# Kernel tuning notes

Measured on AMD Instinct MI355X. Metric: run time of the kernel, lower is better.

Reference implementation:

```python
import jax, jax.numpy as jnp
import numpy as np
from itertools import combinations

B, M = 128, 24
EMB = 16
NEG_SLOPE = 0.01  # torch F.leaky_relu default


def _combo_index():
    # 60 combinations: choose 2 of 4 hole cards x choose 3 of 5 board cards.
    hero = list(combinations(range(4), 2))      # 6
    board = list(combinations(range(5), 3))     # 10
    combos = []
    for h in hero:
        for b in board:
            combos.append([h[0], h[1], 4 + b[0], 4 + b[1], 4 + b[2]])
    return np.asarray(combos, dtype=np.int32)   # (60, 5)

_COMBOS = jnp.asarray(_combo_index())


def setup_inputs() -> dict:
    key = jax.random.key(0)
    ks = jax.random.split(key, 12)
    ranks = jax.random.randint(ks[0], (B, M, 9), 1, 14)   # 1..13
    suits = jax.random.randint(ks[1], (B, M, 9), 1, 5)    # 1..4
    x = jnp.stack([ranks, suits], axis=-1).reshape(B, M, 18).astype(jnp.int64)

    def lin(k, fan_in, fan_out):
        bound = 1.0 / np.sqrt(fan_in)
        kw, kb = jax.random.split(k)
        W = jax.random.uniform(kw, (fan_in, fan_out), minval=-bound, maxval=bound, dtype=jnp.float32)
        b = jax.random.uniform(kb, (fan_out,), minval=-bound, maxval=bound, dtype=jnp.float32)
        return W, b

    card_emb = jax.random.normal(ks[2], (53, EMB), dtype=jnp.float32)
    card_emb = card_emb.at[0].set(0.0)  # padding_idx=0
    hand_W, hand_b = lin(ks[3], 32, 128)
    board_W, board_b = lin(ks[4], 48, 128)
    hidden_W, hidden_b = lin(ks[5], 256, 256)
    out_W, out_b = lin(ks[6], 60 * 256, 256)
    return {"x": x, "card_emb": card_emb,
            "hand_W": hand_W, "hand_b": hand_b,
            "board_W": board_W, "board_b": board_b,
            "hidden_W": hidden_W, "hidden_b": hidden_b,
            "out_W": out_W, "out_b": out_b}


def reference(x, card_emb, hand_W, hand_b, board_W, board_b,
              hidden_W, hidden_b, out_W, out_b):
    act = lambda v: jax.nn.leaky_relu(v, NEG_SLOPE)
    Bx, Mx = x.shape[0], x.shape[1]
    ranks = x[..., 0::2]                       # (B,M,9)
    suits = x[..., 1::2]
    rc = jnp.take(ranks, _COMBOS, axis=-1)     # (B,M,60,5)
    sc = jnp.take(suits, _COMBOS, axis=-1)
    rc = jnp.where(rc > 0, rc - 1, 0)          # ranks -> 0..12
    sc = jnp.where(sc > 0, (sc - 1) * 13, 0)   # suit offset 0/13/26/39
    cards = rc + sc                            # (B,M,60,5) in [0,52)
    emb = card_emb[cards]                      # (B,M,60,5,16)
    hero = emb[..., :2, :].reshape(Bx, Mx, 60, 32)
    board = emb[..., 2:, :].reshape(Bx, Mx, 60, 48)
    hero = act(hero @ hand_W + hand_b)         # (B,M,60,128)
    board = act(board @ board_W + board_b)     # (B,M,60,128)
    h = act(jnp.concatenate([hero, board], axis=-1) @ hidden_W + hidden_b)  # (B,M,60,256)
    flat = h.reshape(Bx, Mx, 60 * 256)         # (B,M,15360)
    return act(flat @ out_W + out_b)           # (B,M,256)
```

## Files before the change

### kernel.cpp

```cpp
#include <hip/hip_runtime.h>
#include <hip/hip_bf16.h>
#include <cstdint>
#include <cstddef>

typedef __hip_bfloat16 bf16;
typedef __attribute__((ext_vector_type(8))) short short8;
typedef __attribute__((ext_vector_type(4))) float floatx4;

#define KO 15360
#define KS 12
#define KSLICE 1280

__device__ __forceinline__ float lrelu(float v) { return v > 0.f ? v : 0.01f * v; }

__device__ __forceinline__ float bflo(unsigned int u) {
  unsigned int x = u << 16; float f; __builtin_memcpy(&f, &x, 4); return f;
}
__device__ __forceinline__ float bfhi(unsigned int u) {
  unsigned int x = u & 0xffff0000u; float f; __builtin_memcpy(&f, &x, 4); return f;
}
__device__ __forceinline__ unsigned int pk2(float lo, float hi) {
  bf16 a = __float2bfloat16(lo), b = __float2bfloat16(hi);
  unsigned short ua, ub;
  __builtin_memcpy(&ua, &a, 2); __builtin_memcpy(&ub, &b, 2);
  return (unsigned int)ua | ((unsigned int)ub << 16);
}
__device__ __forceinline__ unsigned int hpair(unsigned int u, unsigned int v) {
  return pk2(lrelu(bflo(u) + bflo(v)), lrelu(bfhi(u) + bfhi(v)));
}

__device__ __forceinline__ void async_lds16(const bf16* g, bf16* l) {
  __builtin_amdgcn_global_load_lds((__attribute__((address_space(1))) void*)(g),
                                   (__attribute__((address_space(3))) void*)(l),
                                   16, 0, 0);
}

__global__ __launch_bounds__(256) void transpose_k(const float* __restrict__ W,
                                                   bf16* __restrict__ Wt, int K)
{
  __shared__ float tile[64][65];
  const int kb = blockIdx.x * 64;
  const int nb = blockIdx.y * 64;
  const int t = threadIdx.x;
  #pragma unroll
  for (int i = 0; i < 16; ++i) {
    int idx = t + 256 * i;
    int r = idx >> 6, c = idx & 63;
    tile[r][c] = W[(size_t)(kb + r) * 256 + nb + c];
  }
  __syncthreads();
  #pragma unroll
  for (int i = 0; i < 16; ++i) {
    int idx = t + 256 * i;
    int r = idx >> 6, c = idx & 63;
    Wt[(size_t)(nb + r) * K + kb + c] = __float2bfloat16(tile[c][r]);
  }
}

__global__ __launch_bounds__(256) void hb_pack(
    const int* __restrict__ x, const float* __restrict__ card_emb,
    const float* __restrict__ hand_W, const float* __restrict__ hand_b,
    const float* __restrict__ board_W, const float* __restrict__ board_b,
    bf16* __restrict__ Abuf)
{
  static constexpr int H0[6] = {0,0,0,1,1,2};
  static constexpr int H1[6] = {1,2,3,2,3,3};
  static constexpr int B0[10] = {0,0,0,0,0,0,1,1,1,2};
  static constexpr int B1[10] = {1,1,1,2,2,3,2,2,3,3};
  static constexpr int B2[10] = {2,3,4,3,4,4,3,4,4,4};

  __shared__ float wH[32 * 128];
  __shared__ float wB[48 * 128];
  __shared__ float bH[128], bB[128];
  __shared__ float emb[4][9][16];
  __shared__ bf16 At[2][16][264];

  const int t = threadIdx.x;
  const int item0 = blockIdx.x * 4;

  for (int i = t; i < 32 * 128; i += 256) wH[i] = hand_W[i];
  for (int i = t; i < 48 * 128; i += 256) wB[i] = board_W[i];
  if (t < 128) { bH[t] = hand_b[t]; bB[t] = board_b[t]; }
  for (int ii = t; ii < 576; ii += 256) {
    int li = ii / 144, idx = ii - li * 144;
    int ci = idx >> 4, e = idx & 15;
    int rk = x[(item0 + li) * 18 + 2 * ci], st = x[(item0 + li) * 18 + 2 * ci + 1];
    int card = (rk > 0 ? rk - 1 : 0) + (st > 0 ? (st - 1) * 13 : 0);
    emb[li][ci][e] = card_emb[card * 16 + e];
  }
  __syncthreads();

  const int half = t >> 7, j = t & 127;

  for (int pass = 0; pass < 2; ++pass) {
    const int embi = 2 * pass + half;
    {
      bf16 z = __float2bfloat16(0.f);
      #pragma unroll
      for (int p = 0; p < 6; ++p) At[half][p][128 + j] = z;
      #pragma unroll
      for (int b = 0; b < 10; ++b) At[half][6 + b][j] = z;
    }
    float aH[6], aB[10];
    {
      float hb = bH[j], bb = bB[j];
      #pragma unroll
      for (int p = 0; p < 6; ++p) aH[p] = hb;
      #pragma unroll
      for (int b = 0; b < 10; ++b) aB[b] = bb;
    }
    #pragma unroll
    for (int k = 0; k < 16; ++k) {
      float e[9];
      #pragma unroll
      for (int c = 0; c < 9; ++c) e[c] = emb[embi][c][k];
      float w0 = wH[k * 128 + j], w1 = wH[(16 + k) * 128 + j];
      float v0 = wB[k * 128 + j], v1 = wB[(16 + k) * 128 + j], v2 = wB[(32 + k) * 128 + j];
      #pragma unroll
      for (int p = 0; p < 6; ++p)
        aH[p] += e[H0[p]] * w0 + e[H1[p]] * w1;
      #pragma unroll
      for (int b = 0; b < 10; ++b)
        aB[b] += e[4 + B0[b]] * v0 + e[4 + B1[b]] * v1 + e[4 + B2[b]] * v2;
    }
    #pragma unroll
    for (int p = 0; p < 6; ++p) At[half][p][j] = __float2bfloat16(lrelu(aH[p]));
    #pragma unroll
    for (int b = 0; b < 10; ++b) At[half][6 + b][128 + j] = __float2bfloat16(lrelu(aB[b]));
    __syncthreads();

    #pragma unroll
    for (int li2 = 0; li2 < 2; ++li2) {
      #pragma unroll
      for (int cc = 0; cc < 2; ++cc) {
        int c = t + 256 * cc;
        int m = c & 15, kq = (c >> 4) & 3, ks = c >> 6;
        short8 v = *(const short8*)&At[li2][m][ks * 32 + kq * 8];
        *(short8*)(Abuf + (size_t)(item0 + 2 * pass + li2) * 4096 + (size_t)c * 8) = v;
      }
    }
    __syncthreads();
  }
}

__global__ __launch_bounds__(256, 2) void uv_gemm(
    const bf16* __restrict__ Abuf, const bf16* __restrict__ hWt,
    const float* __restrict__ hidden_b, bf16* __restrict__ UV)
{
  const int t = threadIdx.x, w = t >> 6, l = t & 63;
  const int lr = l & 15, quad = l >> 4;

  short8 bfrag[4][8];
  float bias[4];
  #pragma unroll
  for (int tl = 0; tl < 4; ++tl) {
    int n = w * 64 + tl * 16 + lr;
    bias[tl] = hidden_b[n];
    #pragma unroll
    for (int ks = 0; ks < 8; ++ks)
      bfrag[tl][ks] = *(const short8*)(hWt + (size_t)n * 256 + ks * 32 + quad * 8);
  }

  const int i0 = blockIdx.x * 6;
  for (int ii = 0; ii < 6; ++ii) {
    const bf16* ab = Abuf + (size_t)(i0 + ii) * 4096;
    short8 a[8];
    #pragma unroll
    for (int ks = 0; ks < 8; ++ks)
      a[ks] = *(const short8*)(ab + (size_t)(ks * 64 + l) * 8);

    floatx4 acc[4];
    floatx4 zero = {0.f, 0.f, 0.f, 0.f};
    #pragma unroll
    for (int i = 0; i < 4; ++i) acc[i] = zero;
    #pragma unroll
    for (int ks = 0; ks < 8; ++ks)
      #pragma unroll
      for (int tl = 0; tl < 4; ++tl)
        acc[tl] = __builtin_amdgcn_mfma_f32_16x16x32_bf16(a[ks], bfrag[tl][ks], acc[tl], 0, 0, 0);

    bf16* dst = UV + (size_t)(i0 + ii) * 4096;
    #pragma unroll
    for (int tl = 0; tl < 4; ++tl) {
      int n = w * 64 + tl * 16 + lr;
      #pragma unroll
      for (int r = 0; r < 4; ++r) {
        int m = quad * 4 + r;
        float v = acc[tl][r] + (m >= 6 ? bias[tl] : 0.f);
        dst[m * 256 + n] = __float2bfloat16(v);
      }
    }
  }
}

__global__ __launch_bounds__(256, 2) void out_gemm(
    const bf16* __restrict__ UV, const bf16* __restrict__ Wt,
    float* __restrict__ pbuf)
{
  __shared__ bf16 As[64 * 64];
  __shared__ bf16 Bs[256 * 64];

  const int t = threadIdx.x;
  const int w = t >> 6, l = t & 63, lr = l & 15, quad = l >> 4;
  const int m0 = blockIdx.x * 64;
  const int ks0 = blockIdx.y * KSLICE;
  const int ar = t >> 2, ac = t & 3;

  const bf16* rowp[8];
  {
    int rl = l >> 3, j = (l & 7) ^ rl;
    #pragma unroll
    for (int q = 0; q < 8; ++q)
      rowp[q] = Wt + (size_t)(w * 64 + 8 * q + rl) * KO + ks0 + j * 8;
  }
  bf16* BsW = &Bs[w * 4096];

  floatx4 acc[16];
  floatx4 zero = {0.f, 0.f, 0.f, 0.f};
  #pragma unroll
  for (int i = 0; i < 16; ++i) acc[i] = zero;

  uint4 cu0, cu1, cv0, cv1;
  {
    const int combo = ks0 >> 8;
    const int urow = combo / 10, vrow = 6 + (combo - urow * 10);
    const int c0 = ks0 & 255;
    const bf16* ub = UV + ((size_t)(m0 + ar) * 16 + urow) * 256 + c0 + ac * 16;
    const bf16* vb = UV + ((size_t)(m0 + ar) * 16 + vrow) * 256 + c0 + ac * 16;
    cu0 = *(const uint4*)ub;  cu1 = *(const uint4*)(ub + 8);
    cv0 = *(const uint4*)vb;  cv1 = *(const uint4*)(vb + 8);
  }

  for (int it = 0; it < KSLICE / 64; ++it) {
    __syncthreads();

    #pragma unroll
    for (int q = 0; q < 8; ++q)
      async_lds16(rowp[q] + it * 64, BsW + q * 512);

    {
      uint4 h0, h1;
      h0.x = hpair(cu0.x, cv0.x); h0.y = hpair(cu0.y, cv0.y);
      h0.z = hpair(cu0.z, cv0.z); h0.w = hpair(cu0.w, cv0.w);
      h1.x = hpair(cu1.x, cv1.x); h1.y = hpair(cu1.y, cv1.y);
      h1.z = hpair(cu1.z, cv1.z); h1.w = hpair(cu1.w, cv1.w);
      int jA0 = (2 * ac) ^ (ar & 7);
      int jA1 = (2 * ac + 1) ^ (ar & 7);
      *(uint4*)&As[ar * 64 + jA0 * 8] = h0;
      *(uint4*)&As[ar * 64 + jA1 * 8] = h1;
    }

    __syncthreads();

    if (it + 1 < KSLICE / 64) {
      const int gk2 = ks0 + (it + 1) * 64;
      const int combo = gk2 >> 8;
      const int urow = combo / 10, vrow = 6 + (combo - urow * 10);
      const int c0 = gk2 & 255;
      const bf16* ub = UV + ((size_t)(m0 + ar) * 16 + urow) * 256 + c0 + ac * 16;
      const bf16* vb = UV + ((size_t)(m0 + ar) * 16 + vrow) * 256 + c0 + ac * 16;
      cu0 = *(const uint4*)ub;  cu1 = *(const uint4*)(ub + 8);
      cv0 = *(const uint4*)vb;  cv1 = *(const uint4*)(vb + 8);
    }

    #pragma unroll
    for (int ks = 0; ks < 2; ++ks) {
      short8 af[4], bfr[4];
      #pragma unroll
      for (int i = 0; i < 4; ++i) {
        int row = i * 16 + lr;
        int jp = (4 * ks + quad) ^ (row & 7);
        af[i] = *(const short8*)&As[row * 64 + jp * 8];
      }
      #pragma unroll
      for (int j = 0; j < 4; ++j) {
        int row = w * 64 + j * 16 + lr;
        int jp = (4 * ks + quad) ^ (row & 7);
        bfr[j] = *(const short8*)&Bs[row * 64 + jp * 8];
      }
      #pragma unroll
      for (int i = 0; i < 4; ++i)
        #pragma unroll
        for (int j = 0; j < 4; ++j)
          acc[i * 4 + j] = __builtin_amdgcn_mfma_f32_16x16x32_bf16(af[i], bfr[j], acc[i * 4 + j], 0, 0, 0);
    }
  }

  float* dst = pbuf + (((size_t)blockIdx.y * 48 + blockIdx.x) * 4 + w) * 4096 + l;
  #pragma unroll
  for (int a = 0; a < 16; ++a)
    #pragma unroll
    for (int r = 0; r < 4; ++r)
      dst[(a * 4 + r) * 64] = acc[a][r];
}

__global__ __launch_bounds__(256) void reduce_bias(
    const float* __restrict__ pbuf, const float* __restrict__ outb,
    float* __restrict__ out, int slice_stride)
{
  int idx = blockIdx.x * 256 + threadIdx.x;
  float s = 0.f;
  #pragma unroll
  for (int k = 0; k < KS; ++k) s += pbuf[idx + (size_t)k * slice_stride];
  int l = idx & 63, q = (idx >> 6) & 63, w = (idx >> 12) & 3, bx = idx >> 14;
  int a = q >> 2, r = q & 3, i = a >> 2, tl = a & 3;
  int lr = l & 15, quad = l >> 4;
  int m = bx * 64 + i * 16 + quad * 4 + r;
  int n = w * 64 + tl * 16 + lr;
  out[(size_t)m * 256 + n] = lrelu(s + outb[n]);
}

extern "C" void kernel_launch(void* const* d_in, const int* in_sizes, int n_in,
                              void* d_out, int out_size, void* d_ws, size_t ws_size,
                              hipStream_t stream)
{
  const int*   x        = (const int*)  d_in[0];
  const float* card_emb = (const float*)d_in[1];
  const float* hand_W   = (const float*)d_in[2];
  const float* hand_b   = (const float*)d_in[3];
  const float* board_W  = (const float*)d_in[4];
  const float* board_b  = (const float*)d_in[5];
  const float* hidden_W = (const float*)d_in[6];
  const float* hidden_b = (const float*)d_in[7];
  const float* out_W    = (const float*)d_in[8];
  const float* out_b    = (const float*)d_in[9];
  float* out = (float*)d_out;

  const int NI = in_sizes[0] / 18;

  char* ws = (char*)d_ws;
  bf16* hWt  = (bf16*)ws;
  bf16* oWt  = (bf16*)(ws + 131072);
  bf16* UV   = (bf16*)(ws + 131072 + 7864320);
  bf16* Abuf = (bf16*)(ws + 131072 + 7864320 + (size_t)NI * 8192);
  float* pbuf = (float*)Abuf;

  transpose_k<<<dim3(4, 4),   256, 0, stream>>>(hidden_W, hWt, 256);
  transpose_k<<<dim3(240, 4), 256, 0, stream>>>(out_W,    oWt, KO);
  hb_pack<<<NI / 4, 256, 0, stream>>>(x, card_emb, hand_W, hand_b,
                                      board_W, board_b, Abuf);
  uv_gemm<<<NI / 6, 256, 0, stream>>>(Abuf, hWt, hidden_b, UV);
  out_gemm<<<dim3(NI / 64, KS), 256, 0, stream>>>(UV, oWt, pbuf);
  reduce_bias<<<NI, 256, 0, stream>>>(pbuf, out_b, out, NI * 256);
}
```

Measured before the change: 180.7 us.

## Fuse hand/board pack with UV GEMM, double-buffer out GEMM, vectorise reduce

Merges the hand/board embedding kernel with the hidden-layer UV GEMM so the packed activations feed MFMAs directly from LDS and skip a global round trip. The output GEMM gets double-buffered LDS tiles, so the next B tile and A build overlap the current MFMAs, and the split-K count goes from 12 to 16 slices. The reduction kernel now handles four elements per thread with float4 loads and stores. Costs are more LDS in out_gemm, since the doubled buffers cut occupancy, and more partial sums to reduce.

```diff
diff --git a/kernel.cpp b/kernel.cpp
--- a/kernel.cpp
+++ b/kernel.cpp
@@ -8,8 +8,9 @@
 typedef __attribute__((ext_vector_type(4))) float floatx4;
 
 #define KO 15360
-#define KS 12
-#define KSLICE 1280
+#define KS 16
+#define KSLICE 960
+#define NIT (KSLICE / 64)
 
 __device__ __forceinline__ float lrelu(float v) { return v > 0.f ? v : 0.01f * v; }
 
@@ -57,11 +58,12 @@
   }
 }
 
-__global__ __launch_bounds__(256) void hb_pack(
+__global__ __launch_bounds__(256, 2) void hb_uv(
     const int* __restrict__ x, const float* __restrict__ card_emb,
     const float* __restrict__ hand_W, const float* __restrict__ hand_b,
     const float* __restrict__ board_W, const float* __restrict__ board_b,
-    bf16* __restrict__ Abuf)
+    const bf16* __restrict__ hWt, const float* __restrict__ hidden_b,
+    bf16* __restrict__ UV)
 {
   static constexpr int H0[6] = {0,0,0,1,1,2};
   static constexpr int H1[6] = {1,2,3,2,3,3};
@@ -76,10 +78,22 @@
   __shared__ bf16 At[2][16][264];
 
   const int t = threadIdx.x;
+  const int w = t >> 6, l = t & 63, lr = l & 15, quad = l >> 4;
   const int item0 = blockIdx.x * 4;
 
-  for (int i = t; i < 32 * 128; i += 256) wH[i] = hand_W[i];
-  for (int i = t; i < 48 * 128; i += 256) wB[i] = board_W[i];
+  short8 bfrag[4][8];
+  float bias[4];
+  #pragma unroll
+  for (int tl = 0; tl < 4; ++tl) {
+    int n = w * 64 + tl * 16 + lr;
+    bias[tl] = hidden_b[n];
+    #pragma unroll
+    for (int ks = 0; ks < 8; ++ks)
+      bfrag[tl][ks] = *(const short8*)(hWt + (size_t)n * 256 + ks * 32 + quad * 8);
+  }
+
+  for (int i = t * 4; i < 4096; i += 1024) *(float4*)&wH[i] = *(const float4*)&hand_W[i];
+  for (int i = t * 4; i < 6144; i += 1024) *(float4*)&wB[i] = *(const float4*)&board_W[i];
   if (t < 128) { bH[t] = hand_b[t]; bB[t] = board_b[t]; }
   for (int ii = t; ii < 576; ii += 256) {
     int li = ii / 144, idx = ii - li * 144;
@@ -93,6 +107,7 @@
   const int half = t >> 7, j = t & 127;
 
   for (int pass = 0; pass < 2; ++pass) {
+    if (pass) __syncthreads();
     const int embi = 2 * pass + half;
     {
       bf16 z = __float2bfloat16(0.f);
@@ -130,75 +145,71 @@
     __syncthreads();
 
     #pragma unroll
-    for (int li2 = 0; li2 < 2; ++li2) {
-      #pragma unroll
-      for (int cc = 0; cc < 2; ++cc) {
-        int c = t + 256 * cc;
-        int m = c & 15, kq = (c >> 4) & 3, ks = c >> 6;
-        short8 v = *(const short8*)&At[li2][m][ks * 32 + kq * 8];
-        *(short8*)(Abuf + (size_t)(item0 + 2 * pass + li2) * 4096 + (size_t)c * 8) = v;
+    for (int li = 0; li < 2; ++li) {
+      short8 a[8];
+      #pragma unroll
+      for (int ks = 0; ks < 8; ++ks)
+        a[ks] = *(const short8*)&At[li][lr][ks * 32 + quad * 8];
+
+      floatx4 acc[4];
+      floatx4 zero = {0.f, 0.f, 0.f, 0.f};
+      #pragma unroll
+      for (int i = 0; i < 4; ++i) acc[i] = zero;
+      #pragma unroll
+      for (int ks = 0; ks < 8; ++ks)
+        #pragma unroll
+        for (int tl = 0; tl < 4; ++tl)
+          acc[tl] = __builtin_amdgcn_mfma_f32_16x16x32_bf16(a[ks], bfrag[tl][ks], acc[tl], 0, 0, 0);
+
+      bf16* dst = UV + (size_t)(item0 + 2 * pass + li) * 4096;
+      #pragma unroll
+      for (int tl = 0; tl < 4; ++tl) {
+        int n = w * 64 + tl * 16 + lr;
+        #pragma unroll
+        for (int r = 0; r < 4; ++r) {
+          int m = quad * 4 + r;
+          float v = acc[tl][r] + (m >= 6 ? bias[tl] : 0.f);
+          dst[m * 256 + n] = __float2bfloat16(v);
+        }
       }
     }
-    __syncthreads();
-  }
-}
-
-__global__ __launch_bounds__(256, 2) void uv_gemm(
-    const bf16* __restrict__ Abuf, const bf16* __restrict__ hWt,
-    const float* __restrict__ hidden_b, bf16* __restrict__ UV)
-{
-  const int t = threadIdx.x, w = t >> 6, l = t & 63;
-  const int lr = l & 15, quad = l >> 4;
-
-  short8 bfrag[4][8];
-  float bias[4];
-  #pragma unroll
-  for (int tl = 0; tl < 4; ++tl) {
-    int n = w * 64 + tl * 16 + lr;
-    bias[tl] = hidden_b[n];
-    #pragma unroll
-    for (int ks = 0; ks < 8; ++ks)
-      bfrag[tl][ks] = *(const short8*)(hWt + (size_t)n * 256 + ks * 32 + quad * 8);
-  }
-
-  const int i0 = blockIdx.x * 6;
-  for (int ii = 0; ii < 6; ++ii) {
-    const bf16* ab = Abuf + (size_t)(i0 + ii) * 4096;
-    short8 a[8];
-    #pragma unroll
-    for (int ks = 0; ks < 8; ++ks)
-      a[ks] = *(const short8*)(ab + (size_t)(ks * 64 + l) * 8);
-
-    floatx4 acc[4];
-    floatx4 zero = {0.f, 0.f, 0.f, 0.f};
-    #pragma unroll
-    for (int i = 0; i < 4; ++i) acc[i] = zero;
-    #pragma unroll
-    for (int ks = 0; ks < 8; ++ks)
-      #pragma unroll
-      for (int tl = 0; tl < 4; ++tl)
-        acc[tl] = __builtin_amdgcn_mfma_f32_16x16x32_bf16(a[ks], bfrag[tl][ks], acc[tl], 0, 0, 0);
-
-    bf16* dst = UV + (size_t)(i0 + ii) * 4096;
-    #pragma unroll
-    for (int tl = 0; tl < 4; ++tl) {
-      int n = w * 64 + tl * 16 + lr;
-      #pragma unroll
-      for (int r = 0; r < 4; ++r) {
-        int m = quad * 4 + r;
-        float v = acc[tl][r] + (m >= 6 ? bias[tl] : 0.f);
-        dst[m * 256 + n] = __float2bfloat16(v);
-      }
-    }
-  }
+  }
+}
+
+__device__ __forceinline__ void uv_fetch(const bf16* __restrict__ UV, int m0, int ar,
+                                         int ac, int ks0, int it,
+                                         uint4& u0, uint4& u1, uint4& v0, uint4& v1)
+{
+  const int gk = ks0 + it * 64;
+  const int combo = gk >> 8;
+  const int urow = combo / 10, vrow = 6 + (combo - urow * 10);
+  const int c0 = gk & 255;
+  const bf16* ub = UV + ((size_t)(m0 + ar) * 16 + urow) * 256 + c0 + ac * 16;
+  const bf16* vb = UV + ((size_t)(m0 + ar) * 16 + vrow) * 256 + c0 + ac * 16;
+  u0 = *(const uint4*)ub;  u1 = *(const uint4*)(ub + 8);
+  v0 = *(const uint4*)vb;  v1 = *(const uint4*)(vb + 8);
+}
+
+__device__ __forceinline__ void build_As(bf16* __restrict__ AsBuf, int ar, int ac,
+                                         uint4 u0, uint4 u1, uint4 v0, uint4 v1)
+{
+  uint4 h0, h1;
+  h0.x = hpair(u0.x, v0.x); h0.y = hpair(u0.y, v0.y);
+  h0.z = hpair(u0.z, v0.z); h0.w = hpair(u0.w, v0.w);
+  h1.x = hpair(u1.x, v1.x); h1.y = hpair(u1.y, v1.y);
+  h1.z = hpair(u1.z, v1.z); h1.w = hpair(u1.w, v1.w);
+  int jA0 = (2 * ac) ^ (ar & 7);
+  int jA1 = (2 * ac + 1) ^ (ar & 7);
+  *(uint4*)&AsBuf[ar * 64 + jA0 * 8] = h0;
+  *(uint4*)&AsBuf[ar * 64 + jA1 * 8] = h1;
 }
 
 __global__ __launch_bounds__(256, 2) void out_gemm(
     const bf16* __restrict__ UV, const bf16* __restrict__ Wt,
     float* __restrict__ pbuf)
 {
-  __shared__ bf16 As[64 * 64];
-  __shared__ bf16 Bs[256 * 64];
+  __shared__ bf16 As[2][64 * 64];
+  __shared__ bf16 Bs[2][256 * 64];
 
   const int t = threadIdx.x;
   const int w = t >> 6, l = t & 63, lr = l & 15, quad = l >> 4;
@@ -213,54 +224,34 @@
     for (int q = 0; q < 8; ++q)
       rowp[q] = Wt + (size_t)(w * 64 + 8 * q + rl) * KO + ks0 + j * 8;
   }
-  bf16* BsW = &Bs[w * 4096];
 
   floatx4 acc[16];
   floatx4 zero = {0.f, 0.f, 0.f, 0.f};
   #pragma unroll
   for (int i = 0; i < 16; ++i) acc[i] = zero;
 
-  uint4 cu0, cu1, cv0, cv1;
+  #pragma unroll
+  for (int q = 0; q < 8; ++q)
+    async_lds16(rowp[q], &Bs[0][w * 4096 + q * 512]);
   {
-    const int combo = ks0 >> 8;
-    const int urow = combo / 10, vrow = 6 + (combo - urow * 10);
-    const int c0 = ks0 & 255;
-    const bf16* ub = UV + ((size_t)(m0 + ar) * 16 + urow) * 256 + c0 + ac * 16;
-    const bf16* vb = UV + ((size_t)(m0 + ar) * 16 + vrow) * 256 + c0 + ac * 16;
-    cu0 = *(const uint4*)ub;  cu1 = *(const uint4*)(ub + 8);
-    cv0 = *(const uint4*)vb;  cv1 = *(const uint4*)(vb + 8);
-  }
-
-  for (int it = 0; it < KSLICE / 64; ++it) {
+    uint4 u0, u1, v0, v1;
+    uv_fetch(UV, m0, ar, ac, ks0, 0, u0, u1, v0, v1);
+    build_As(As[0], ar, ac, u0, u1, v0, v1);
+  }
+  uint4 nu0, nu1, nv0, nv1;
+  uv_fetch(UV, m0, ar, ac, ks0, 1, nu0, nu1, nv0, nv1);
+
+  for (int it = 0; it < NIT; ++it) {
+    const int cur = it & 1, nxt = cur ^ 1;
     __syncthreads();
 
-    #pragma unroll
-    for (int q = 0; q < 8; ++q)
-      async_lds16(rowp[q] + it * 64, BsW + q * 512);
-
-    {
-      uint4 h0, h1;
-      h0.x = hpair(cu0.x, cv0.x); h0.y = hpair(cu0.y, cv0.y);
-      h0.z = hpair(cu0.z, cv0.z); h0.w = hpair(cu0.w, cv0.w);
-      h1.x = hpair(cu1.x, cv1.x); h1.y = hpair(cu1.y, cv1.y);
-      h1.z = hpair(cu1.z, cv1.z); h1.w = hpair(cu1.w, cv1.w);
-      int jA0 = (2 * ac) ^ (ar & 7);
-      int jA1 = (2 * ac + 1) ^ (ar & 7);
-      *(uint4*)&As[ar * 64 + jA0 * 8] = h0;
-      *(uint4*)&As[ar * 64 + jA1 * 8] = h1;
-    }
-
-    __syncthreads();
-
-    if (it + 1 < KSLICE / 64) {
-      const int gk2 = ks0 + (it + 1) * 64;
-      const int combo = gk2 >> 8;
-      const int urow = combo / 10, vrow = 6 + (combo - urow * 10);
-      const int c0 = gk2 & 255;
-      const bf16* ub = UV + ((size_t)(m0 + ar) * 16 + urow) * 256 + c0 + ac * 16;
-      const bf16* vb = UV + ((size_t)(m0 + ar) * 16 + vrow) * 256 + c0 + ac * 16;
-      cu0 = *(const uint4*)ub;  cu1 = *(const uint4*)(ub + 8);
-      cv0 = *(const uint4*)vb;  cv1 = *(const uint4*)(vb + 8);
+    if (it + 1 < NIT) {
+      #pragma unroll
+      for (int q = 0; q < 8; ++q)
+        async_lds16(rowp[q] + (it + 1) * 64, &Bs[nxt][w * 4096 + q * 512]);
+      build_As(As[nxt], ar, ac, nu0, nu1, nv0, nv1);
+      if (it + 2 < NIT)
+        uv_fetch(UV, m0, ar, ac, ks0, it + 2, nu0, nu1, nv0, nv1);
     }
 
     #pragma unroll
@@ -270,13 +261,13 @@
       for (int i = 0; i < 4; ++i) {
         int row = i * 16 + lr;
         int jp = (4 * ks + quad) ^ (row & 7);
-        af[i] = *(const short8*)&As[row * 64 + jp * 8];
+        af[i] = *(const short8*)&As[cur][row * 64 + jp * 8];
       }
       #pragma unroll
       for (int j = 0; j < 4; ++j) {
         int row = w * 64 + j * 16 + lr;
         int jp = (4 * ks + quad) ^ (row & 7);
-        bfr[j] = *(const short8*)&Bs[row * 64 + jp * 8];
+        bfr[j] = *(const short8*)&Bs[cur][row * 64 + jp * 8];
       }
       #pragma unroll
       for (int i = 0; i < 4; ++i)
@@ -298,16 +289,24 @@
     const float* __restrict__ pbuf, const float* __restrict__ outb,
     float* __restrict__ out, int slice_stride)
 {
-  int idx = blockIdx.x * 256 + threadIdx.x;
-  float s = 0.f;
-  #pragma unroll
-  for (int k = 0; k < KS; ++k) s += pbuf[idx + (size_t)k * slice_stride];
-  int l = idx & 63, q = (idx >> 6) & 63, w = (idx >> 12) & 3, bx = idx >> 14;
+  int i4 = blockIdx.x * 256 + threadIdx.x;
+  int idx = i4 * 4;
+  float4 s = *(const float4*)&pbuf[idx];
+  #pragma unroll
+  for (int k = 1; k < KS; ++k) {
+    float4 v = *(const float4*)&pbuf[idx + (size_t)k * slice_stride];
+    s.x += v.x; s.y += v.y; s.z += v.z; s.w += v.w;
+  }
+  int l = idx & 63, q = (idx >> 6) & 63, w2 = (idx >> 12) & 3, bx = idx >> 14;
   int a = q >> 2, r = q & 3, i = a >> 2, tl = a & 3;
   int lr = l & 15, quad = l >> 4;
   int m = bx * 64 + i * 16 + quad * 4 + r;
-  int n = w * 64 + tl * 16 + lr;
-  out[(size_t)m * 256 + n] = lrelu(s + outb[n]);
+  int n = w2 * 64 + tl * 16 + lr;
+  float4 b = *(const float4*)&outb[n];
+  float4 rr;
+  rr.x = lrelu(s.x + b.x); rr.y = lrelu(s.y + b.y);
+  rr.z = lrelu(s.z + b.z); rr.w = lrelu(s.w + b.w);
+  *(float4*)&out[(size_t)m * 256 + n] = rr;
 }
 
 extern "C" void kernel_launch(void* const* d_in, const int* in_sizes, int n_in,
@@ -332,14 +331,12 @@
   bf16* hWt  = (bf16*)ws;
   bf16* oWt  = (bf16*)(ws + 131072);
   bf16* UV   = (bf16*)(ws + 131072 + 7864320);
-  bf16* Abuf = (bf16*)(ws + 131072 + 7864320 + (size_t)NI * 8192);
-  float* pbuf = (float*)Abuf;
+  float* pbuf = (float*)(ws + 131072 + 7864320 + (size_t)NI * 8192);
 
   transpose_k<<<dim3(4, 4),   256, 0, stream>>>(hidden_W, hWt, 256);
   transpose_k<<<dim3(240, 4), 256, 0, stream>>>(out_W,    oWt, KO);
-  hb_pack<<<NI / 4, 256, 0, stream>>>(x, card_emb, hand_W, hand_b,
-                                      board_W, board_b, Abuf);
-  uv_gemm<<<NI / 6, 256, 0, stream>>>(Abuf, hWt, hidden_b, UV);
+  hb_uv<<<NI / 4, 256, 0, stream>>>(x, card_emb, hand_W, hand_b,
+                                    board_W, board_b, hWt, hidden_b, UV);
   out_gemm<<<dim3(NI / 64, KS), 256, 0, stream>>>(UV, oWt, pbuf);
-  reduce_bias<<<NI, 256, 0, stream>>>(pbuf, out_b, out, NI * 256);
-}
+  reduce_bias<<<NI / 4, 256, 0, stream>>>(pbuf, out_b, out, NI * 256);
+}
```

After: 218.3 us. 20.8% more time.

## Retune split-K, swizzle out_gemm blocks, prepack hidden weights, vectorize loads and reduce

Applied to the files above, without the earlier changes.

The output GEMM now uses 16 K-slices of 960 instead of 12 of 1280, on a flattened 1D grid. Block indices are remapped so neighbouring blocks share M tiles across K-slices, which should improve L2 reuse of UV and the weights. The hidden weights are prepacked straight into the MFMA fragment layout, so uv_gemm gets contiguous per-lane loads. hb_pack weight staging uses float4 loads, and the split-K reduction reads, biases and writes four floats per thread. In exchange, the partial-sum buffer grows and there is more reduction traffic, and the new block count may give a worse wave tail on the CUs.

```diff
diff --git a/kernel.cpp b/kernel.cpp
--- a/kernel.cpp
+++ b/kernel.cpp
@@ -8,8 +8,9 @@
 typedef __attribute__((ext_vector_type(4))) float floatx4;
 
 #define KO 15360
-#define KS 12
-#define KSLICE 1280
+#define KS 16
+#define KSLICE 960
+#define NIT (KSLICE / 64)
 
 __device__ __forceinline__ float lrelu(float v) { return v > 0.f ? v : 0.01f * v; }
 
@@ -57,6 +58,29 @@
   }
 }
 
+__global__ __launch_bounds__(256) void pack_hidden(const float* __restrict__ W,
+                                                   bf16* __restrict__ P)
+{
+  __shared__ float Lt[4096];
+  const int g = blockIdx.x, t = threadIdx.x;
+  for (int i = t; i < 4096; i += 256)
+    Lt[i] = W[(size_t)(i >> 4) * 256 + g * 16 + (i & 15)];
+  __syncthreads();
+  #pragma unroll
+  for (int cc = 0; cc < 2; ++cc) {
+    int c = t + 256 * cc;
+    int ks = c >> 6, l = c & 63, lr = l & 15, quad = l >> 4;
+    short8 v;
+    #pragma unroll
+    for (int j = 0; j < 8; ++j) {
+      bf16 b = __float2bfloat16(Lt[(ks * 32 + quad * 8 + j) * 16 + lr]);
+      short s; __builtin_memcpy(&s, &b, 2);
+      v[j] = s;
+    }
+    *(short8*)(P + ((size_t)(g * 8 + ks) * 64 + l) * 8) = v;
+  }
+}
+
 __global__ __launch_bounds__(256) void hb_pack(
     const int* __restrict__ x, const float* __restrict__ card_emb,
     const float* __restrict__ hand_W, const float* __restrict__ hand_b,
@@ -78,8 +102,8 @@
   const int t = threadIdx.x;
   const int item0 = blockIdx.x * 4;
 
-  for (int i = t; i < 32 * 128; i += 256) wH[i] = hand_W[i];
-  for (int i = t; i < 48 * 128; i += 256) wB[i] = board_W[i];
+  for (int i = t * 4; i < 4096; i += 1024) *(float4*)&wH[i] = *(const float4*)&hand_W[i];
+  for (int i = t * 4; i < 6144; i += 1024) *(float4*)&wB[i] = *(const float4*)&board_W[i];
   if (t < 128) { bH[t] = hand_b[t]; bB[t] = board_b[t]; }
   for (int ii = t; ii < 576; ii += 256) {
     int li = ii / 144, idx = ii - li * 144;
@@ -93,6 +117,7 @@
   const int half = t >> 7, j = t & 127;
 
   for (int pass = 0; pass < 2; ++pass) {
+    if (pass) __syncthreads();
     const int embi = 2 * pass + half;
     {
       bf16 z = __float2bfloat16(0.f);
@@ -144,7 +169,7 @@
 }
 
 __global__ __launch_bounds__(256, 2) void uv_gemm(
-    const bf16* __restrict__ Abuf, const bf16* __restrict__ hWt,
+    const bf16* __restrict__ Abuf, const bf16* __restrict__ hWtp,
     const float* __restrict__ hidden_b, bf16* __restrict__ UV)
 {
   const int t = threadIdx.x, w = t >> 6, l = t & 63;
@@ -154,11 +179,10 @@
   float bias[4];
   #pragma unroll
   for (int tl = 0; tl < 4; ++tl) {
-    int n = w * 64 + tl * 16 + lr;
-    bias[tl] = hidden_b[n];
+    bias[tl] = hidden_b[w * 64 + tl * 16 + lr];
     #pragma unroll
     for (int ks = 0; ks < 8; ++ks)
-      bfrag[tl][ks] = *(const short8*)(hWt + (size_t)n * 256 + ks * 32 + quad * 8);
+      bfrag[tl][ks] = *(const short8*)(hWtp + ((size_t)((w * 4 + tl) * 8 + ks) * 64 + l) * 8);
   }
 
   const int i0 = blockIdx.x * 6;
@@ -193,6 +217,20 @@
   }
 }
 
+__device__ __forceinline__ void uv_fetch(const bf16* __restrict__ UV, int m0, int ar,
+                                         int ac, int ks0, int it,
+                                         uint4& u0, uint4& u1, uint4& v0, uint4& v1)
+{
+  const int gk = ks0 + it * 64;
+  const int combo = gk >> 8;
+  const int urow = combo / 10, vrow = 6 + (combo - urow * 10);
+  const int c0 = gk & 255;
+  const bf16* ub = UV + ((size_t)(m0 + ar) * 16 + urow) * 256 + c0 + ac * 16;
+  const bf16* vb = UV + ((size_t)(m0 + ar) * 16 + vrow) * 256 + c0 + ac * 16;
+  u0 = *(const uint4*)ub;  u1 = *(const uint4*)(ub + 8);
+  v0 = *(const uint4*)vb;  v1 = *(const uint4*)(vb + 8);
+}
+
 __global__ __launch_bounds__(256, 2) void out_gemm(
     const bf16* __restrict__ UV, const bf16* __restrict__ Wt,
     float* __restrict__ pbuf)
@@ -201,9 +239,12 @@
   __shared__ bf16 Bs[256 * 64];
 
   const int t = threadIdx.x;
+  const int id = blockIdx.x;
+  const int by = ((id & 7) << 1) | ((id >> 3) & 1);
+  const int bx = id >> 4;
   const int w = t >> 6, l = t & 63, lr = l & 15, quad = l >> 4;
-  const int m0 = blockIdx.x * 64;
-  const int ks0 = blockIdx.y * KSLICE;
+  const int m0 = bx * 64;
+  const int ks0 = by * KSLICE;
   const int ar = t >> 2, ac = t & 3;
 
   const bf16* rowp[8];
@@ -221,17 +262,9 @@
   for (int i = 0; i < 16; ++i) acc[i] = zero;
 
   uint4 cu0, cu1, cv0, cv1;
-  {
-    const int combo = ks0 >> 8;
-    const int urow = combo / 10, vrow = 6 + (combo - urow * 10);
-    const int c0 = ks0 & 255;
-    const bf16* ub = UV + ((size_t)(m0 + ar) * 16 + urow) * 256 + c0 + ac * 16;
-    const bf16* vb = UV + ((size_t)(m0 + ar) * 16 + vrow) * 256 + c0 + ac * 16;
-    cu0 = *(const uint4*)ub;  cu1 = *(const uint4*)(ub + 8);
-    cv0 = *(const uint4*)vb;  cv1 = *(const uint4*)(vb + 8);
-  }
-
-  for (int it = 0; it < KSLICE / 64; ++it) {
+  uv_fetch(UV, m0, ar, ac, ks0, 0, cu0, cu1, cv0, cv1);
+
+  for (int it = 0; it < NIT; ++it) {
     __syncthreads();
 
     #pragma unroll
@@ -252,16 +285,8 @@
 
     __syncthreads();
 
-    if (it + 1 < KSLICE / 64) {
-      const int gk2 = ks0 + (it + 1) * 64;
-      const int combo = gk2 >> 8;
-      const int urow = combo / 10, vrow = 6 + (combo - urow * 10);
-      const int c0 = gk2 & 255;
-      const bf16* ub = UV + ((size_t)(m0 + ar) * 16 + urow) * 256 + c0 + ac * 16;
-      const bf16* vb = UV + ((size_t)(m0 + ar) * 16 + vrow) * 256 + c0 + ac * 16;
-      cu0 = *(const uint4*)ub;  cu1 = *(const uint4*)(ub + 8);
-      cv0 = *(const uint4*)vb;  cv1 = *(const uint4*)(vb + 8);
-    }
+    if (it + 1 < NIT)
+      uv_fetch(UV, m0, ar, ac, ks0, it + 1, cu0, cu1, cv0, cv1);
 
     #pragma unroll
     for (int ks = 0; ks < 2; ++ks) {
@@ -286,7 +311,7 @@
     }
   }
 
-  float* dst = pbuf + (((size_t)blockIdx.y * 48 + blockIdx.x) * 4 + w) * 4096 + l;
+  float* dst = pbuf + (((size_t)by * 48 + bx) * 4 + w) * 4096 + l;
   #pragma unroll
   for (int a = 0; a < 16; ++a)
     #pragma unroll
@@ -298,16 +323,24 @@
     const float* __restrict__ pbuf, const float* __restrict__ outb,
     float* __restrict__ out, int slice_stride)
 {
-  int idx = blockIdx.x * 256 + threadIdx.x;
-  float s = 0.f;
-  #pragma unroll
-  for (int k = 0; k < KS; ++k) s += pbuf[idx + (size_t)k * slice_stride];
-  int l = idx & 63, q = (idx >> 6) & 63, w = (idx >> 12) & 3, bx = idx >> 14;
+  int i4 = blockIdx.x * 256 + threadIdx.x;
+  int idx = i4 * 4;
+  float4 s = *(const float4*)&pbuf[idx];
+  #pragma unroll
+  for (int k = 1; k < KS; ++k) {
+    float4 v = *(const float4*)&pbuf[idx + (size_t)k * slice_stride];
+    s.x += v.x; s.y += v.y; s.z += v.z; s.w += v.w;
+  }
+  int l = idx & 63, q = (idx >> 6) & 63, w2 = (idx >> 12) & 3, bx = idx >> 14;
   int a = q >> 2, r = q & 3, i = a >> 2, tl = a & 3;
   int lr = l & 15, quad = l >> 4;
   int m = bx * 64 + i * 16 + quad * 4 + r;
-  int n = w * 64 + tl * 16 + lr;
-  out[(size_t)m * 256 + n] = lrelu(s + outb[n]);
+  int n = w2 * 64 + tl * 16 + lr;
+  float4 b = *(const float4*)&outb[n];
+  float4 rr;
+  rr.x = lrelu(s.x + b.x); rr.y = lrelu(s.y + b.y);
+  rr.z = lrelu(s.z + b.z); rr.w = lrelu(s.w + b.w);
+  *(float4*)&out[(size_t)m * 256 + n] = rr;
 }
 
 extern "C" void kernel_launch(void* const* d_in, const int* in_sizes, int n_in,
@@ -329,17 +362,17 @@
   const int NI = in_sizes[0] / 18;
 
   char* ws = (char*)d_ws;
-  bf16* hWt  = (bf16*)ws;
+  bf16* hWtp = (bf16*)ws;
   bf16* oWt  = (bf16*)(ws + 131072);
   bf16* UV   = (bf16*)(ws + 131072 + 7864320);
   bf16* Abuf = (bf16*)(ws + 131072 + 7864320 + (size_t)NI * 8192);
   float* pbuf = (float*)Abuf;
 
-  transpose_k<<<dim3(4, 4),   256, 0, stream>>>(hidden_W, hWt, 256);
-  transpose_k<<<dim3(240, 4), 256, 0, stream>>>(out_W,    oWt, KO);
+  pack_hidden<<<16, 256, 0, stream>>>(hidden_W, hWtp);
+  transpose_k<<<dim3(240, 4), 256, 0, stream>>>(out_W, oWt, KO);
   hb_pack<<<NI / 4, 256, 0, stream>>>(x, card_emb, hand_W, hand_b,
                                       board_W, board_b, Abuf);
-  uv_gemm<<<NI / 6, 256, 0, stream>>>(Abuf, hWt, hidden_b, UV);
-  out_gemm<<<dim3(NI / 64, KS), 256, 0, stream>>>(UV, oWt, pbuf);
-  reduce_bias<<<NI, 256, 0, stream>>>(pbuf, out_b, out, NI * 256);
-}
+  uv_gemm<<<NI / 6, 256, 0, stream>>>(Abuf, hWtp, hidden_b, UV);
+  out_gemm<<<NI / 64 * KS, 256, 0, stream>>>(UV, oWt, pbuf);
+  reduce_bias<<<NI / 4, 256, 0, stream>>>(pbuf, out_b, out, NI * 256);
+}
```

Result: faster. 170.6 us (-5.6%).
